# Optimization experiments

Hardware: AMD Instinct MI355X
Metric: run time of the kernel (lower is better)

## Reference

```python
import math
import jax, jax.numpy as jnp
import numpy as np

B, T_BI, D_BI = 64, 3000, 128
T_SW, D_SW = 375, 192
T_S1, D_S1 = 188, 192
N_FIRES = 300          # static fire count (target_lengths all = 300 -> beta = 1, ceil(sum)=300)
D_MODEL = 512
SCALE = 4.0            # scale_factor
EPS_LN = 1e-5


def _cif_integrate(h, alpha, thr, n_fires):
    """Vectorized CIF: cumsum + two scatter-adds (matches torch _cif_forward).
    h [B,T,D], alpha [B,T], thr [B,1] -> [B,n_fires,D]."""
    Bq, T, D = h.shape
    a = alpha / thr                       # normalize so boundaries sit at integers
    c = jnp.cumsum(a, axis=1)
    prev = c - a
    kp = jnp.floor(prev)
    kc = jnp.floor(c)
    fired = kc > kp                       # frame crosses a token boundary
    w_hi = jnp.where(fired, (c - kc) * thr, 0.0)          # leftover into new token
    w_lo = jnp.where(fired, (kp + 1.0 - prev) * thr, alpha)  # portion completing old token
    ip = jnp.clip(kp.astype(jnp.int32), 0, n_fires - 1)
    ic = jnp.clip(kc.astype(jnp.int32), 0, n_fires - 1)
    bidx = jnp.broadcast_to(jnp.arange(Bq)[:, None], (Bq, T))
    out = jnp.zeros((Bq, n_fires, D), h.dtype)
    out = out.at[bidx, ip].add(w_lo[..., None] * h)
    out = out.at[bidx, ic].add(w_hi[..., None] * h)
    return out


def _interp(src, t_cont, t_bi):
    """Linear interp of src [B,Ts,D] at continuous fire times t_cont [B,N] (given on the T_bi grid)."""
    Bq, Ts, D = src.shape
    t = t_cont * Ts / t_bi
    lo = jnp.clip(t.astype(jnp.int32), 0, Ts - 2)
    w = (t - lo.astype(t.dtype))[..., None]
    idx_lo = jnp.broadcast_to(lo[..., None], (Bq, t.shape[1], D))
    g_lo = jnp.take_along_axis(src, idx_lo, axis=1)
    g_hi = jnp.take_along_axis(src, idx_lo + 1, axis=1)
    return (1.0 - w) * g_lo + w * g_hi


def _forward(fire_signal, acoustic_src, acoustic_src_s1, conv_w, ln_g, ln_b, wp_w, wp_b,
             film_s0_w, film_s0_b, film_s1_w, film_s1_b, tproj_w, tproj_b,
             aproj_w, aproj_b, bproj_w, bproj_b, target_lengths):
    Bq, T_bi, _ = fire_signal.shape
    # 1) weight predictor: depthwise conv (k=1, no bias) -> LN -> Linear -> sigmoid
    x = fire_signal * conv_w                                   # depthwise 1x1 conv
    mu = jnp.mean(x, axis=-1, keepdims=True)
    var = jnp.var(x, axis=-1, keepdims=True)
    xn = (x - mu) * jax.lax.rsqrt(var + EPS_LN) * ln_g + ln_b
    alpha = SCALE * jax.nn.sigmoid(xn @ wp_w + wp_b)           # [B,T]
    tgt = target_lengths.astype(alpha.dtype)
    qty_loss = jnp.mean(jnp.abs(jnp.sum(alpha, axis=1) - tgt))
    # training-mode alpha normalization (sum alpha_cif == target)
    sum_a = jnp.clip(jnp.sum(alpha, axis=1, keepdims=True), 1e-8)
    alpha_cif = alpha * (tgt[:, None] / sum_a)
    # dynamic threshold beta = sum / ceil(sum)  (== 1 here since targets are integers)
    sum_cif = jnp.sum(alpha_cif, axis=1)
    ceil_sum = jax.lax.stop_gradient(jnp.clip(jnp.ceil(sum_cif), 1.0))
    thr = (sum_cif / ceil_sum)[:, None]                        # [B,1]
    # 2) CIF integration of temporal channel
    acoustic_temporal = _cif_integrate(fire_signal, alpha_cif, thr, N_FIRES)  # [B,N,128]
    # continuous fire times
    cum = jnp.cumsum(alpha_cif, axis=1)
    thresholds = jnp.arange(1, N_FIRES + 1, dtype=alpha.dtype)[None, :] * thr  # [B,N]
    ff = jax.vmap(jnp.searchsorted)(cum, thresholds)
    ff = jnp.minimum(ff, T_bi - 1)
    t_lo = jnp.maximum(ff - 1, 0)
    cum_at = jnp.take_along_axis(cum, t_lo, axis=1)
    a_at = jnp.take_along_axis(alpha_cif, ff, axis=1)
    t_cont = t_lo.astype(alpha.dtype) + (thresholds - cum_at) / jnp.clip(a_at, 1e-8)
    t_cont = jnp.clip(t_cont, 0.0, T_bi - 1)
    # 3) S0 pitch channel: interp + FiLM
    acoustic_pitch = _interp(acoustic_src, t_cont, T_bi)       # [B,N,192]
    film0 = acoustic_temporal @ film_s0_w + film_s0_b
    g0, b0 = jnp.split(film0, 2, axis=-1)
    pitch_mod = g0 * acoustic_pitch + b0
    # 4) project + combine
    embs = (acoustic_temporal @ tproj_w + tproj_b) + (pitch_mod @ aproj_w + aproj_b)
    # S1 beat channel
    acoustic_beat = _interp(acoustic_src_s1, t_cont, T_bi)     # [B,N,192]
    film1 = acoustic_temporal @ film_s1_w + film_s1_b
    g1, b1 = jnp.split(film1, 2, axis=-1)
    beat_mod = g1 * acoustic_beat + b1
    embs = embs + (beat_mod @ bproj_w + bproj_b)
    return embs, alpha, qty_loss


def setup_inputs() -> dict:
    key = jax.random.key(0)
    ks = jax.random.split(key, 14)
    # weight_proj bias init per module: alpha_init = target_fires/encoder_len
    p = min((128.0 / 3000.0) / SCALE, 0.99)
    wp_bias = math.log(p / (1.0 - p))
    f32 = jnp.float32
    return {
        "fire_signal": jax.random.normal(ks[0], (B, T_BI, D_BI), f32),
        "acoustic_src": jax.random.normal(ks[1], (B, T_SW, D_SW), f32),
        "acoustic_src_s1": jax.random.normal(ks[2], (B, T_S1, D_S1), f32),
        "target_lengths": jnp.full((B,), N_FIRES, jnp.int32),
        "conv_w": 1.0 + 0.1 * jax.random.normal(ks[3], (D_BI,), f32),
        "ln_g": jnp.ones((D_BI,), f32),
        "ln_b": jnp.zeros((D_BI,), f32),
        "wp_w": 0.02 * jax.random.normal(ks[4], (D_BI,), f32),
        "wp_b": jnp.asarray(wp_bias, f32),
        "film_s0_w": 0.02 * jax.random.normal(ks[5], (D_BI, 2 * D_SW), f32),
        "film_s0_b": jnp.concatenate([jnp.ones((D_SW,), f32), jnp.zeros((D_SW,), f32)]),
        "film_s1_w": 0.02 * jax.random.normal(ks[6], (D_BI, 2 * D_S1), f32),
        "film_s1_b": jnp.concatenate([jnp.ones((D_S1,), f32), jnp.zeros((D_S1,), f32)]),
        "tproj_w": 0.02 * jax.random.normal(ks[7], (D_BI, D_MODEL), f32),
        "tproj_b": jnp.zeros((D_MODEL,), f32),
        "aproj_w": 0.02 * jax.random.normal(ks[8], (D_SW, D_MODEL), f32),
        "aproj_b": jnp.zeros((D_MODEL,), f32),
        "bproj_w": 0.02 * jax.random.normal(ks[9], (D_S1, D_MODEL), f32),
        "bproj_b": jnp.zeros((D_MODEL,), f32),
    }


def reference(fire_signal, acoustic_src, acoustic_src_s1, target_lengths, conv_w, ln_g, ln_b,
              wp_w, wp_b, film_s0_w, film_s0_b, film_s1_w, film_s1_b, tproj_w, tproj_b,
              aproj_w, aproj_b, bproj_w, bproj_b):
    return _forward(fire_signal, acoustic_src, acoustic_src_s1, conv_w, ln_g, ln_b, wp_w, wp_b,
                    film_s0_w, film_s0_b, film_s1_w, film_s1_b, tproj_w, tproj_b,
                    aproj_w, aproj_b, bproj_w, bproj_b, target_lengths)
```

## Files before the change

kernel.cpp:

```cpp
#include <hip/hip_runtime.h>
#include <math.h>

#define BQ 64
#define TBI 3000
#define DBI 128
#define TSW 375
#define TS1 188
#define DSW 192
#define NF 300
#define DMODEL 512
#define EPSLN 1e-5f

typedef __bf16 bf16x8 __attribute__((ext_vector_type(8)));
typedef float f32x4 __attribute__((ext_vector_type(4)));

__device__ __forceinline__ unsigned short f2bf(float f) {
    unsigned u = __float_as_uint(f);
    unsigned r = (u + 0x7FFFu + ((u >> 16) & 1u)) >> 16;
    return (unsigned short)r;
}

__global__ __launch_bounds__(256) void k_alpha2(
    const float* __restrict__ fs, const float* __restrict__ conv_w,
    const float* __restrict__ ln_g, const float* __restrict__ ln_b,
    const float* __restrict__ wp_w, const float* __restrict__ wp_b,
    float* __restrict__ alpha_out)
{
    int wave = threadIdx.x >> 6, lane = threadIdx.x & 63;
    int l = lane & 31;
    long g = (long)blockIdx.x * 8 + wave * 2 + (lane >> 5);
    const float* row = fs + g * DBI;
    float4 f  = *(const float4*)&row[4 * l];
    float4 cw = *(const float4*)&conv_w[4 * l];
    float4 x; x.x = f.x * cw.x; x.y = f.y * cw.y; x.z = f.z * cw.z; x.w = f.w * cw.w;
    float s = x.x + x.y + x.z + x.w;
    for (int m = 16; m >= 1; m >>= 1) s += __shfl_xor(s, m, 64);
    float mu = s * (1.0f / 128.0f);
    float4 d; d.x = x.x - mu; d.y = x.y - mu; d.z = x.z - mu; d.w = x.w - mu;
    float q = d.x * d.x + d.y * d.y + d.z * d.z + d.w * d.w;
    for (int m = 16; m >= 1; m >>= 1) q += __shfl_xor(q, m, 64);
    float var = q * (1.0f / 128.0f);
    float rs = rsqrtf(var + EPSLN);
    float4 lg = *(const float4*)&ln_g[4 * l];
    float4 lb = *(const float4*)&ln_b[4 * l];
    float4 wp = *(const float4*)&wp_w[4 * l];
    float z = (d.x * rs * lg.x + lb.x) * wp.x + (d.y * rs * lg.y + lb.y) * wp.y
            + (d.z * rs * lg.z + lb.z) * wp.z + (d.w * rs * lg.w + lb.w) * wp.w;
    for (int m = 16; m >= 1; m >>= 1) z += __shfl_xor(z, m, 64);
    z += wp_b[0];
    float a = 4.0f / (1.0f + expf(-z));
    if (l == 0) alpha_out[g] = a;
}

__global__ __launch_bounds__(1024) void k_scan3(
    const float* __restrict__ alpha, const int* __restrict__ tlen,
    float2* __restrict__ params, float* __restrict__ qtyo,
    float2* __restrict__ c2, float* __restrict__ tcont, int* __restrict__ ffout)
{
    __shared__ float2 sc[TBI];
    __shared__ float2 part[2][1024];
    __shared__ double red[1024];
    int b = blockIdx.x, tid = threadIdx.x;
    const float* ar = alpha + (long)b * TBI;
    double s = 0.0;
    for (int t = tid; t < TBI; t += 1024) s += (double)ar[t];
    red[tid] = s; __syncthreads();
    for (int d = 512; d >= 1; d >>= 1) { if (tid < d) red[tid] += red[tid + d]; __syncthreads(); }
    double sum_a = red[0]; __syncthreads();
    double tgt = (double)tlen[b];
    double sa = sum_a < 1e-8 ? 1e-8 : sum_a;
    float r = (float)(tgt / sa);
    double s2 = 0.0;
    for (int t = tid; t < TBI; t += 1024) s2 += (double)(ar[t] * r);
    red[tid] = s2; __syncthreads();
    for (int d = 512; d >= 1; d >>= 1) { if (tid < d) red[tid] += red[tid + d]; __syncthreads(); }
    float sum_cif = (float)red[0];
    float cs = ceilf(sum_cif); if (cs < 1.0f) cs = 1.0f;
    float thr = sum_cif / cs;
    float rthr = 1.0f / thr;
    if (tid == 0) {
        params[b] = make_float2(r, thr);
        atomicAdd(qtyo, (float)fabs(sum_a - tgt) * (1.0f / (float)BQ));
    }
    int base = tid * 3;
    float2 run = make_float2(0.f, 0.f);
    if (base < TBI) {
        for (int j = 0; j < 3; ++j) {
            int t = base + j;
            float ac = ar[t] * r;
            run.x += ac * rthr; run.y += ac;
            sc[t] = run;
        }
    }
    part[0][tid] = (base < TBI) ? run : make_float2(0.f, 0.f);
    __syncthreads();
    int srcb = 0;
    for (int d = 1; d < 1024; d <<= 1) {
        float2 v = part[srcb][tid];
        if (tid >= d) { float2 u = part[srcb][tid - d]; v.x += u.x; v.y += u.y; }
        part[srcb ^ 1][tid] = v;
        srcb ^= 1;
        __syncthreads();
    }
    if (base < TBI && tid > 0) {
        float2 off = part[srcb][tid - 1];
        for (int j = 0; j < 3; ++j) { sc[base + j].x += off.x; sc[base + j].y += off.y; }
    }
    __syncthreads();
    for (int t = tid; t < TBI; t += 1024) {
        float ac = ar[t] * r;
        c2[(long)b * TBI + t] = make_float2(sc[t].x, ac);
    }
    if (tid < NF) {
        float v = (float)(tid + 1) * thr;
        int lo = 0, hi = TBI;
        while (lo < hi) { int mid = (lo + hi) >> 1; if (sc[mid].y < v) lo = mid + 1; else hi = mid; }
        int ff = lo; if (ff > TBI - 1) ff = TBI - 1;
        ffout[b * NF + tid] = ff;
        int tl = ff - 1; if (tl < 0) tl = 0;
        float cum_at = sc[tl].y;
        float a_at = ar[ff] * r;
        if (a_at < 1e-8f) a_at = 1e-8f;
        float tc = (float)tl + (v - cum_at) / a_at;
        tc = fminf(fmaxf(tc, 0.0f), (float)(TBI - 1));
        tcont[b * NF + tid] = tc;
    }
}

#define TPW 3
__global__ __launch_bounds__(256) void k_cif3(
    const float* __restrict__ fs, const float2* __restrict__ c2,
    const int* __restrict__ ffA, const float2* __restrict__ params,
    float* __restrict__ at)
{
    int wid = threadIdx.x >> 6, lane = threadIdx.x & 63;
    int wg = blockIdx.x * 4 + wid;
    int b = wg / 100, slot = wg - b * 100;
    int j0 = slot * TPW;
    const int* ffb = ffA + b * NF;
    int t0 = (j0 == 0) ? 0 : ffb[j0 - 1];
    int tE = (slot == 99) ? (TBI - 1) : ffb[j0 + TPW - 1];
    float thr = params[b].y;
    float rthr = 1.0f / thr;
    const float2* cb = c2 + (long)b * TBI;
    const float* fb = fs + (long)b * TBI * DBI;
    float* ab = at + (long)b * NF * DBI;
    int nw = j0;
    int cur = -1;
    float a0 = 0.f, a1 = 0.f;
    #define FLUSH() do { \
        if (cur >= j0 && cur < j0 + TPW) { \
            while (nw < cur) { *(float2*)&ab[nw * DBI + 2 * lane] = make_float2(0.f, 0.f); ++nw; } \
            *(float2*)&ab[cur * DBI + 2 * lane] = make_float2(a0, a1); nw = cur + 1; \
        } } while (0)
    for (int t = t0; t <= tE; ++t) {
        float2 v = cb[t];
        float2 h = *(const float2*)&fb[(long)t * DBI + 2 * lane];
        float c = v.x, ac = v.y;
        float av = ac * rthr;
        float prev = c - av;
        float kp = floorf(prev), kc = floorf(c);
        bool fired = kc > kp;
        float w_lo = fired ? (kp + 1.0f - prev) * thr : ac;
        float w_hi = fired ? (c - kc) * thr : 0.0f;
        int ip = (int)kp; if (ip > NF - 1) ip = NF - 1; if (ip < 0) ip = 0;
        int ic = (int)kc; if (ic > NF - 1) ic = NF - 1; if (ic < 0) ic = 0;
        if (ip != cur) { FLUSH(); cur = ip; a0 = 0.f; a1 = 0.f; }
        a0 += w_lo * h.x; a1 += w_lo * h.y;
        if (fired) {
            if (ic != cur) { FLUSH(); cur = ic; a0 = 0.f; a1 = 0.f; }
            a0 += w_hi * h.x; a1 += w_hi * h.y;
        }
    }
    FLUSH();
    while (nw < j0 + TPW) { *(float2*)&ab[nw * DBI + 2 * lane] = make_float2(0.f, 0.f); ++nw; }
    #undef FLUSH
}

__global__ __launch_bounds__(256) void k_prep2(
    const float* __restrict__ f0w, const float* __restrict__ f1w,
    const float* __restrict__ tw, const float* __restrict__ aw, const float* __restrict__ bw,
    const float* __restrict__ f0b, const float* __restrict__ f1b,
    const float* __restrict__ tb, const float* __restrict__ apb, const float* __restrict__ bpb,
    unsigned short* __restrict__ Wg, unsigned short* __restrict__ Wb,
    unsigned short* __restrict__ W2,
    float* __restrict__ gbias, float* __restrict__ bbias, float* __restrict__ bias2,
    float* __restrict__ qtyo)
{
    if (blockIdx.x == 1216) {
        for (int c = threadIdx.x; c < 512; c += 256) {
            if (c < 384) {
                gbias[c] = c < 192 ? f0b[c] : f1b[c - 192];
                bbias[c] = c < 192 ? f0b[c + 192] : f1b[c - 192 + 192];
            }
            bias2[c] = tb[c] + apb[c] + bpb[c];
        }
        if (threadIdx.x == 0) qtyo[0] = 0.f;
        return;
    }
    int i = blockIdx.x * 256 + threadIdx.x;
    if (i < 49152) {
        int j = i & 7, lane = (i >> 3) & 63, kt = (i >> 9) & 3, nt = i >> 11;
        int k = kt * 32 + (lane >> 4) * 8 + j;
        int n = nt * 16 + (lane & 15);
        float g, b;
        if (n < 192) { g = f0w[k * 384 + n];         b = f0w[k * 384 + n + 192]; }
        else         { g = f1w[k * 384 + (n - 192)]; b = f1w[k * 384 + (n - 192) + 192]; }
        Wg[i] = f2bf(g); Wb[i] = f2bf(b);
    } else {
        int ii = i - 49152;
        int j = ii & 7, lane = (ii >> 3) & 63, kt = (ii >> 9) & 15, nt = ii >> 13;
        int k = kt * 32 + (lane >> 4) * 8 + j;
        int n = nt * 16 + (lane & 15);
        float v;
        if (k < 128)      v = tw[k * 512 + n];
        else if (k < 320) v = aw[(k - 128) * 512 + n];
        else              v = bw[(k - 320) * 512 + n];
        W2[ii] = f2bf(v);
    }
}

#define EROWS 16
__global__ __launch_bounds__(512, 6) void k_emb5(
    const float* __restrict__ at, const float* __restrict__ tcont,
    const float* __restrict__ src0, const float* __restrict__ src1,
    const unsigned short* __restrict__ Wg, const unsigned short* __restrict__ Wb,
    const unsigned short* __restrict__ W2,
    const float* __restrict__ gbias, const float* __restrict__ bbias,
    const float* __restrict__ bias2, float* __restrict__ embs)
{
    __shared__ __align__(16) unsigned short X[EROWS][520];
    __shared__ float s_w0[EROWS], s_w1[EROWS];
    __shared__ int s_lo0[EROWS], s_lo1[EROWS], s_b[EROWS];
    int tid = threadIdx.x;
    int wave = tid >> 6, lane = tid & 63;
    long r0 = (long)blockIdx.x * EROWS;
    {
        int r = tid >> 5, k4 = (tid & 31) * 4;
        float4 v = *(const float4*)&at[(r0 + r) * DBI + k4];
        X[r][k4 + 0] = f2bf(v.x); X[r][k4 + 1] = f2bf(v.y);
        X[r][k4 + 2] = f2bf(v.z); X[r][k4 + 3] = f2bf(v.w);
    }
    if (tid < EROWS) {
        long g = r0 + tid;
        s_b[tid] = (int)(g / NF);
        float tc = tcont[g];
        float t0 = tc * ((float)TSW / 3000.0f);
        int lo0 = (int)t0; if (lo0 > TSW - 2) lo0 = TSW - 2; if (lo0 < 0) lo0 = 0;
        s_lo0[tid] = lo0; s_w0[tid] = t0 - (float)lo0;
        float t1 = tc * ((float)TS1 / 3000.0f);
        int lo1 = (int)t1; if (lo1 > TS1 - 2) lo1 = TS1 - 2; if (lo1 < 0) lo1 = 0;
        s_lo1[tid] = lo1; s_w1[tid] = t1 - (float)lo1;
    }
    __syncthreads();
    int mrow = lane & 15, quad = lane >> 4;
    for (int nt = wave; nt < 24; nt += 8) {
        f32x4 ag = {0,0,0,0}, ab = {0,0,0,0};
        #pragma unroll
        for (int kt = 0; kt < 4; ++kt) {
            bf16x8 a = *(const bf16x8*)&X[mrow][kt * 32 + quad * 8];
            bf16x8 bg = *(const bf16x8*)&Wg[(((nt * 4 + kt) * 64) + lane) * 8];
            bf16x8 bb = *(const bf16x8*)&Wb[(((nt * 4 + kt) * 64) + lane) * 8];
            ag = __builtin_amdgcn_mfma_f32_16x16x32_bf16(a, bg, ag, 0, 0, 0);
            ab = __builtin_amdgcn_mfma_f32_16x16x32_bf16(a, bb, ab, 0, 0, 0);
        }
        int c = nt * 16 + mrow;
        bool sel = c >= DSW;
        int cc = sel ? c - DSW : c;
        const float* S = sel ? src1 : src0;
        int Ts = sel ? TS1 : TSW;
        float gb = gbias[c], bbv = bbias[c];
        #pragma unroll
        for (int q = 0; q < 4; ++q) {
            int r = quad * 4 + q;
            int b = s_b[r];
            int lo = sel ? s_lo1[r] : s_lo0[r];
            float w = sel ? s_w1[r] : s_w0[r];
            const float* Sp = S + ((long)b * Ts + lo) * DSW + cc;
            float pv = (1.0f - w) * Sp[0] + w * Sp[DSW];
            X[r][128 + c] = f2bf((ag[q] + gb) * pv + (ab[q] + bbv));
        }
    }
    __syncthreads();
    f32x4 acc[4];
    #pragma unroll
    for (int n = 0; n < 4; ++n) acc[n] = (f32x4){0, 0, 0, 0};
    for (int kt = 0; kt < 16; ++kt) {
        bf16x8 a = *(const bf16x8*)&X[mrow][kt * 32 + quad * 8];
        #pragma unroll
        for (int n = 0; n < 4; ++n) {
            int nt = wave * 4 + n;
            bf16x8 bfv = *(const bf16x8*)&W2[((nt * 16 + kt) * 64 + lane) * 8];
            acc[n] = __builtin_amdgcn_mfma_f32_16x16x32_bf16(a, bfv, acc[n], 0, 0, 0);
        }
    }
    #pragma unroll
    for (int n = 0; n < 4; ++n) {
        int cbase = (wave * 4 + n) * 16 + mrow;
        float bv = bias2[cbase];
        #pragma unroll
        for (int q = 0; q < 4; ++q)
            embs[(r0 + quad * 4 + q) * DMODEL + cbase] = acc[n][q] + bv;
    }
}

extern "C" void kernel_launch(void* const* d_in, const int* in_sizes, int n_in,
                              void* d_out, int out_size, void* d_ws, size_t ws_size,
                              hipStream_t stream)
{
    const float* fs     = (const float*)d_in[0];
    const float* src0   = (const float*)d_in[1];
    const float* src1   = (const float*)d_in[2];
    const int*   tlen   = (const int*)d_in[3];
    const float* conv_w = (const float*)d_in[4];
    const float* ln_g   = (const float*)d_in[5];
    const float* ln_b   = (const float*)d_in[6];
    const float* wp_w   = (const float*)d_in[7];
    const float* wp_b   = (const float*)d_in[8];
    const float* f0w    = (const float*)d_in[9];
    const float* f0b    = (const float*)d_in[10];
    const float* f1w    = (const float*)d_in[11];
    const float* f1b    = (const float*)d_in[12];
    const float* tw     = (const float*)d_in[13];
    const float* tb     = (const float*)d_in[14];
    const float* aw     = (const float*)d_in[15];
    const float* apb    = (const float*)d_in[16];
    const float* bw     = (const float*)d_in[17];
    const float* bpb    = (const float*)d_in[18];

    float* embs  = (float*)d_out;
    float* alpha = embs + (long)BQ * NF * DMODEL;
    float* qtyo  = alpha + (long)BQ * TBI;

    char* ws = (char*)d_ws;
    size_t off = 0;
    float*  at     = (float*)(ws + off);  off += 9830400;
    float2* c2     = (float2*)(ws + off); off += 1536000;
    float*  tcont  = (float*)(ws + off);  off += 76800;
    int*    ffA    = (int*)(ws + off);    off += 76800;
    float2* params = (float2*)(ws + off); off += 512;
    unsigned short* Wg = (unsigned short*)(ws + off); off += 98304;
    unsigned short* Wb = (unsigned short*)(ws + off); off += 98304;
    unsigned short* W2 = (unsigned short*)(ws + off); off += 524288;
    float* gbias = (float*)(ws + off); off += 1536;
    float* bbias = (float*)(ws + off); off += 1536;
    float* bias2 = (float*)(ws + off); off += 2048;

    k_prep2<<<1217, 256, 0, stream>>>(f0w, f1w, tw, aw, bw, f0b, f1b, tb, apb, bpb,
                                      Wg, Wb, W2, gbias, bbias, bias2, qtyo);
    k_alpha2<<<(BQ * TBI) / 8, 256, 0, stream>>>(fs, conv_w, ln_g, ln_b, wp_w, wp_b, alpha);
    k_scan3<<<BQ, 1024, 0, stream>>>(alpha, tlen, params, qtyo, c2, tcont, ffA);
    k_cif3<<<(BQ * 100) / 4, 256, 0, stream>>>(fs, c2, ffA, params, at);
    k_emb5<<<(BQ * NF) / EROWS, 512, 0, stream>>>(at, tcont, src0, src1,
                                                  Wg, Wb, W2, gbias, bbias, bias2, embs);
}
```

Before: 275.2 us.

## Split FiLM+GEMM into separate kernels with register-resident weights; wave-level scan

The fused FiLM-plus-projection kernel is split in two. The FiLM kernel writes the bf16 activation tile to a workspace buffer in MFMA fragment layout, and a new persistent GEMM kernel keeps each wave's weight column tile in registers while looping over row tiles, prefetching the next A fragments. This removes the repeated global reads of W2 per 16-row block. It costs an extra launch and a write then re-read of about 19.7 MB of intermediate activations. Separately, the per-batch scan's shared-memory tree reductions and Hillis-Steele scan are replaced with wave shuffle reductions and scans, which cuts the number of barriers.

Measured after the change: 285.7 us. +3.8%, slower.

```diff
diff --git a/kernel.cpp b/kernel.cpp
--- a/kernel.cpp
+++ b/kernel.cpp
@@ -52,59 +52,67 @@
     if (l == 0) alpha_out[g] = a;
 }
 
-__global__ __launch_bounds__(1024) void k_scan3(
+__global__ __launch_bounds__(1024) void k_scan4(
     const float* __restrict__ alpha, const int* __restrict__ tlen,
     float2* __restrict__ params, float* __restrict__ qtyo,
     float2* __restrict__ c2, float* __restrict__ tcont, int* __restrict__ ffout)
 {
     __shared__ float2 sc[TBI];
-    __shared__ float2 part[2][1024];
-    __shared__ double red[1024];
+    __shared__ double wsum[16];
+    __shared__ float2 wpart[16];
     int b = blockIdx.x, tid = threadIdx.x;
+    int wid = tid >> 6, lane = tid & 63;
     const float* ar = alpha + (long)b * TBI;
     double s = 0.0;
     for (int t = tid; t < TBI; t += 1024) s += (double)ar[t];
-    red[tid] = s; __syncthreads();
-    for (int d = 512; d >= 1; d >>= 1) { if (tid < d) red[tid] += red[tid + d]; __syncthreads(); }
-    double sum_a = red[0]; __syncthreads();
+    for (int m = 32; m >= 1; m >>= 1) s += __shfl_xor(s, m, 64);
+    if (lane == 0) wsum[wid] = s;
+    __syncthreads();
+    double sum_a = 0.0;
+    #pragma unroll
+    for (int i = 0; i < 16; ++i) sum_a += wsum[i];
     double tgt = (double)tlen[b];
     double sa = sum_a < 1e-8 ? 1e-8 : sum_a;
     float r = (float)(tgt / sa);
+    __syncthreads();
     double s2 = 0.0;
     for (int t = tid; t < TBI; t += 1024) s2 += (double)(ar[t] * r);
-    red[tid] = s2; __syncthreads();
-    for (int d = 512; d >= 1; d >>= 1) { if (tid < d) red[tid] += red[tid + d]; __syncthreads(); }
-    float sum_cif = (float)red[0];
+    for (int m = 32; m >= 1; m >>= 1) s2 += __shfl_xor(s2, m, 64);
+    if (lane == 0) wsum[wid] = s2;
+    __syncthreads();
+    double tot2 = 0.0;
+    #pragma unroll
+    for (int i = 0; i < 16; ++i) tot2 += wsum[i];
+    float sum_cif = (float)tot2;
     float cs = ceilf(sum_cif); if (cs < 1.0f) cs = 1.0f;
     float thr = sum_cif / cs;
     float rthr = 1.0f / thr;
     if (tid == 0) {
         params[b] = make_float2(r, thr);
-        atomicAdd(qtyo, (float)fabs(sum_a - tgt) * (1.0f / (float)BQ));
+        atomicAdd(qtyo, fabsf((float)(sum_a - tgt)) * (1.0f / (float)BQ));
     }
     int base = tid * 3;
-    float2 run = make_float2(0.f, 0.f);
+    float v0x = 0.f, v0y = 0.f, v1x = 0.f, v1y = 0.f, v2x = 0.f, v2y = 0.f;
     if (base < TBI) {
-        for (int j = 0; j < 3; ++j) {
-            int t = base + j;
-            float ac = ar[t] * r;
-            run.x += ac * rthr; run.y += ac;
-            sc[t] = run;
-        }
-    }
-    part[0][tid] = (base < TBI) ? run : make_float2(0.f, 0.f);
-    __syncthreads();
-    int srcb = 0;
-    for (int d = 1; d < 1024; d <<= 1) {
-        float2 v = part[srcb][tid];
-        if (tid >= d) { float2 u = part[srcb][tid - d]; v.x += u.x; v.y += u.y; }
-        part[srcb ^ 1][tid] = v;
-        srcb ^= 1;
-        __syncthreads();
-    }
-    if (base < TBI && tid > 0) {
-        float2 off = part[srcb][tid - 1];
-        for (int j = 0; j < 3; ++j) { sc[base + j].x += off.x; sc[base + j].y += off.y; }
+        float a0 = ar[base] * r, a1 = ar[base + 1] * r, a2 = ar[base + 2] * r;
+        v0x = a0 * rthr;       v0y = a0;
+        v1x = v0x + a1 * rthr; v1y = v0y + a1;
+        v2x = v1x + a2 * rthr; v2y = v1y + a2;
+    }
+    float tx = v2x, ty = v2y;
+    for (int d = 1; d < 64; d <<= 1) {
+        float ux = __shfl_up(tx, d, 64);
+        float uy = __shfl_up(ty, d, 64);
+        if (lane >= d) { tx += ux; ty += uy; }
+    }
+    if (lane == 63) wpart[wid] = make_float2(tx, ty);
+    __syncthreads();
+    float ox = tx - v2x, oy = ty - v2y;
+    for (int i = 0; i < wid; ++i) { ox += wpart[i].x; oy += wpart[i].y; }
+    if (base < TBI) {
+        sc[base]     = make_float2(ox + v0x, oy + v0y);
+        sc[base + 1] = make_float2(ox + v1x, oy + v1y);
+        sc[base + 2] = make_float2(ox + v2x, oy + v2y);
     }
     __syncthreads();
     for (int t = tid; t < TBI; t += 1024) {
@@ -221,13 +229,12 @@
 }
 
 #define EROWS 16
-__global__ __launch_bounds__(512, 6) void k_emb5(
+__global__ __launch_bounds__(512) void k_film(
     const float* __restrict__ at, const float* __restrict__ tcont,
     const float* __restrict__ src0, const float* __restrict__ src1,
     const unsigned short* __restrict__ Wg, const unsigned short* __restrict__ Wb,
-    const unsigned short* __restrict__ W2,
     const float* __restrict__ gbias, const float* __restrict__ bbias,
-    const float* __restrict__ bias2, float* __restrict__ embs)
+    unsigned short* __restrict__ Xs)
 {
     __shared__ __align__(16) unsigned short X[EROWS][520];
     __shared__ float s_w0[EROWS], s_w1[EROWS];
@@ -282,25 +289,55 @@
         }
     }
     __syncthreads();
-    f32x4 acc[4];
+    long mt = blockIdx.x;
+    int l = tid & 63;
+    int ktb = tid >> 6;
     #pragma unroll
-    for (int n = 0; n < 4; ++n) acc[n] = (f32x4){0, 0, 0, 0};
-    for (int kt = 0; kt < 16; ++kt) {
-        bf16x8 a = *(const bf16x8*)&X[mrow][kt * 32 + quad * 8];
-        #pragma unroll
-        for (int n = 0; n < 4; ++n) {
-            int nt = wave * 4 + n;
-            bf16x8 bfv = *(const bf16x8*)&W2[((nt * 16 + kt) * 64 + lane) * 8];
-            acc[n] = __builtin_amdgcn_mfma_f32_16x16x32_bf16(a, bfv, acc[n], 0, 0, 0);
-        }
-    }
+    for (int i = 0; i < 2; ++i) {
+        int kk = ktb + i * 8;
+        uint4 v = *(const uint4*)&X[l & 15][kk * 32 + (l >> 4) * 8];
+        *(uint4*)&Xs[((mt * 16 + kk) * 64 + l) * 8] = v;
+    }
+}
+
+__global__ __launch_bounds__(512, 4) void k_gemm(
+    const unsigned short* __restrict__ Xs, const unsigned short* __restrict__ W2,
+    const float* __restrict__ bias2, float* __restrict__ embs)
+{
+    int tid = threadIdx.x;
+    int wave = tid >> 6, lane = tid & 63;
+    int ngrp = blockIdx.x & 3, mgrp = blockIdx.x >> 2;
+    int nt = ngrp * 8 + wave;
+    bf16x8 b[16];
     #pragma unroll
-    for (int n = 0; n < 4; ++n) {
-        int cbase = (wave * 4 + n) * 16 + mrow;
-        float bv = bias2[cbase];
+    for (int kt = 0; kt < 16; ++kt)
+        b[kt] = *(const bf16x8*)&W2[((nt * 16 + kt) * 64 + lane) * 8];
+    int col = nt * 16 + (lane & 15);
+    float bv = bias2[col];
+    for (int mt = mgrp; mt < 1200; mt += 128) {
+        const unsigned short* xp = Xs + (long)mt * 16 * 64 * 8;
+        f32x4 acc = {0, 0, 0, 0};
+        bf16x8 a[4];
+        #pragma unroll
+        for (int j = 0; j < 4; ++j) a[j] = *(const bf16x8*)&xp[(j * 64 + lane) * 8];
+        #pragma unroll
+        for (int kb = 0; kb < 16; kb += 4) {
+            bf16x8 an[4];
+            if (kb < 12) {
+                #pragma unroll
+                for (int j = 0; j < 4; ++j)
+                    an[j] = *(const bf16x8*)&xp[((kb + 4 + j) * 64 + lane) * 8];
+            }
+            #pragma unroll
+            for (int j = 0; j < 4; ++j)
+                acc = __builtin_amdgcn_mfma_f32_16x16x32_bf16(a[j], b[kb + j], acc, 0, 0, 0);
+            #pragma unroll
+            for (int j = 0; j < 4; ++j) a[j] = an[j];
+        }
+        int rowb = mt * 16 + (lane >> 4) * 4;
         #pragma unroll
         for (int q = 0; q < 4; ++q)
-            embs[(r0 + quad * 4 + q) * DMODEL + cbase] = acc[n][q] + bv;
+            embs[(long)(rowb + q) * DMODEL + col] = acc[q] + bv;
     }
 }
 
@@ -345,12 +382,14 @@
     float* gbias = (float*)(ws + off); off += 1536;
     float* bbias = (float*)(ws + off); off += 1536;
     float* bias2 = (float*)(ws + off); off += 2048;
+    unsigned short* Xs = (unsigned short*)(ws + off); off += 19660800;
 
     k_prep2<<<1217, 256, 0, stream>>>(f0w, f1w, tw, aw, bw, f0b, f1b, tb, apb, bpb,
                                       Wg, Wb, W2, gbias, bbias, bias2, qtyo);
     k_alpha2<<<(BQ * TBI) / 8, 256, 0, stream>>>(fs, conv_w, ln_g, ln_b, wp_w, wp_b, alpha);
-    k_scan3<<<BQ, 1024, 0, stream>>>(alpha, tlen, params, qtyo, c2, tcont, ffA);
+    k_scan4<<<BQ, 1024, 0, stream>>>(alpha, tlen, params, qtyo, c2, tcont, ffA);
     k_cif3<<<(BQ * 100) / 4, 256, 0, stream>>>(fs, c2, ffA, params, at);
-    k_emb5<<<(BQ * NF) / EROWS, 512, 0, stream>>>(at, tcont, src0, src1,
-                                                  Wg, Wb, W2, gbias, bbias, bias2, embs);
-}
+    k_film<<<(BQ * NF) / EROWS, 512, 0, stream>>>(at, tcont, src0, src1,
+                                                  Wg, Wb, gbias, bbias, Xs);
+    k_gemm<<<512, 512, 0, stream>>>(Xs, W2, bias2, embs);
+}
```
